# Performance work log

Hardware: AMD Instinct MI355X
Metric: run time of the kernel (lower is better)

The kernel has to match this reference:

```python
import jax, jax.numpy as jnp
import numpy as np

H, N, OUT = 1024, 64, 512  # channels, SSM state size, output feats


def posenc3d(f, h, w, channels):
    # standard positional_encodings.PositionalEncoding3D
    ch = int(np.ceil(channels / 6) * 2)  # per-axis channels (342 for 1024)
    inv_freq = jnp.asarray(1.0 / (10000.0 ** (np.arange(0, ch, 2, dtype=np.float32) / ch)))

    def emb(n):
        s = jnp.arange(n, dtype=jnp.float32)[:, None] * inv_freq[None, :]  # (n, ch/2)
        return jnp.stack([jnp.sin(s), jnp.cos(s)], axis=-1).reshape(n, -1)  # interleaved (n, ch)

    ex, ey, ez = emb(f), emb(h), emb(w)
    pe = jnp.zeros((f, h, w, ch * 3), dtype=jnp.float32)
    pe = pe.at[..., :ch].set(ex[:, None, None, :])
    pe = pe.at[..., ch:2 * ch].set(ey[None, :, None, :])
    pe = pe.at[..., 2 * ch:].set(ez[None, None, :, :])
    return pe[..., :channels]  # truncate 3*342=1026 -> 1024


def s4_kernel(log_dt, A_re, A_im, C_re, C_im, L):
    # S4D ZOH kernel: K[h,l] = 2*Re( sum_n C'[h,n] * exp(dt_h*A[h,n]*l) )
    dt = jnp.exp(log_dt)                      # (H,)
    A = A_re + 1j * A_im                      # (H,N)
    C = C_re + 1j * C_im                      # (H,N)
    dtA = dt[:, None] * A                     # (H,N)
    Ct = C * (jnp.exp(dtA) - 1.0) / A         # discretized C' (H,N)
    l = jnp.arange(L, dtype=jnp.float32)

    def body(acc, xs):  # scan over state dim to avoid (H,N,L) materialization
        ct, da = xs  # (H,), (H,)
        return acc + ct[:, None] * jnp.exp(da[:, None] * l), None

    acc0 = jnp.zeros((log_dt.shape[0], L), dtype=jnp.complex64)
    K, _ = jax.lax.scan(body, acc0, (Ct.T, dtA.T))
    return 2.0 * K.real  # (H, L)


def reference(x, log_dt, A_re, A_im, C_re, C_im, D, W_out, b_out):
    bs, ch, f, h, w = x.shape
    L = f * h * w
    u = jnp.transpose(x, (0, 2, 3, 4, 1))                 # bs f h w ch
    u = u + posenc3d(f, h, w, ch)[None]
    u = u.reshape(bs, L, ch)
    v = jnp.transpose(u, (0, 2, 1))                       # (bs, ch, L)
    K = s4_kernel(log_dt, A_re, A_im, C_re, C_im, L)      # (ch, L)
    # causal FFT convolution (pad to 2L)
    Uf = jnp.fft.rfft(v, 2 * L)
    Kf = jnp.fft.rfft(K, 2 * L)
    y = jnp.fft.irfft(Uf * Kf[None], 2 * L)[..., :L]
    y = y + D[None, :, None] * v                          # skip connection
    y = jax.nn.gelu(jnp.transpose(y, (0, 2, 1)))          # (bs, L, ch)
    out = y @ W_out + b_out                               # (bs, L, OUT)
    return jnp.transpose(out, (0, 2, 1)).reshape(bs, W_out.shape[1], f, h, w)


def setup_inputs() -> dict:
    key = jax.random.key(0)
    ks = jax.random.split(key, 6)
    bs, f, h, w = 2, 16, 16, 16
    x = jax.random.normal(ks[0], (bs, H, f, h, w), dtype=jnp.float32)
    # S4D-Lin init
    log_dt = jax.random.uniform(ks[1], (H,), dtype=jnp.float32) * (np.log(0.1) - np.log(0.001)) + np.log(0.001)
    A_re = -0.5 * jnp.ones((H, N), dtype=jnp.float32)
    A_im = jnp.broadcast_to(np.pi * jnp.arange(N, dtype=jnp.float32)[None, :], (H, N)).copy()
    C_re = jax.random.normal(ks[2], (H, N), dtype=jnp.float32) * (0.5 ** 0.5)
    C_im = jax.random.normal(ks[3], (H, N), dtype=jnp.float32) * (0.5 ** 0.5)
    D = jax.random.normal(ks[4], (H,), dtype=jnp.float32)
    W_out = jax.random.normal(ks[5], (H, OUT), dtype=jnp.float32) / np.float32(np.sqrt(H))
    b_out = jnp.zeros((OUT,), dtype=jnp.float32)
    return {"x": x, "log_dt": log_dt, "A_re": A_re, "A_im": A_im, "C_re": C_re,
            "C_im": C_im, "D": D, "W_out": W_out, "b_out": b_out}
```

## Files before the change

kernel.cpp:

```cpp
#include <hip/hip_runtime.h>
#include <cstdint>
#include <cstddef>

#define H_CH 1024
#define OUTF 512
#define LSEQ 4096

typedef __bf16 bf16x8 __attribute__((ext_vector_type(8)));
typedef float floatx4 __attribute__((ext_vector_type(4)));

__device__ __forceinline__ unsigned short f2bf(float f) {
    __bf16 b = (__bf16)f;
    return __builtin_bit_cast(unsigned short, b);
}
__device__ __forceinline__ unsigned int pack2(float a, float b) {
    return (unsigned int)f2bf(a) | ((unsigned int)f2bf(b) << 16);
}
__device__ __forceinline__ float bf2f(unsigned short u) {
    unsigned int x = ((unsigned int)u) << 16;
    return __builtin_bit_cast(float, x);
}
struct c32 { float x, y; };
__device__ __forceinline__ c32 cmul(c32 a, c32 b) {
    return { fmaf(a.x, b.x, -a.y * b.y), fmaf(a.x, b.y, a.y * b.x) };
}
__device__ __forceinline__ c32 cpow16(c32 a, int w) {
    c32 p = {1.f, 0.f};
    if (w) {
        c32 a2 = cmul(a, a), a4 = cmul(a2, a2), a8 = cmul(a4, a4), a16 = cmul(a8, a8);
        p = a16;
        for (int k = 1; k < w; ++k) p = cmul(p, a16);
    }
    return p;
}
__device__ __forceinline__ float gelu_fast(float y) {
    float u = y + 0.044715f * y * y * y;
    float e = __expf(-1.5957691216057308f * u);
    return y * __builtin_amdgcn_rcpf(1.f + e);
}

__global__ __launch_bounds__(256) void coef_kernel(
    const float* __restrict__ log_dt, const float* __restrict__ A_re,
    const float* __restrict__ A_im, const float* __restrict__ C_re,
    const float* __restrict__ C_im, float* __restrict__ coef)
{
    const int i = blockIdx.x * 256 + threadIdx.x;
    const int c = i >> 6;
    double are = A_re[i], aim = A_im[i], cre = C_re[i], cim = C_im[i];
    double dt  = exp((double)log_dt[c]);
    double dar = dt * are, dai = dt * aim;
    double er = exp(dar), cd = cos(dai), sd = sin(dai);
    double lre = er * cd, limm = er * sd;
    double ei = exp(-dar);
    double eQ = exp(64.0 * dar), cQ = cos(64.0 * dai), sQ = sin(64.0 * dai);
    double nre = lre - 1.0, nim = limm;
    double d2  = are * are + aim * aim;
    double qre = (nre * are + nim * aim) / d2;
    double qim = (nim * are - nre * aim) / d2;
    double ctre = cre * qre - cim * qim, ctim = cre * qim + cim * qre;
    float4 w0 = make_float4((float)lre, (float)limm, (float)(ei * cd), (float)(-ei * sd));
    float4 w1 = make_float4((float)(eQ * cQ), (float)(eQ * sQ),
                            (float)(2.0 * ctre), (float)(-2.0 * ctim));
    *(float4*)&coef[(size_t)i * 8]     = w0;
    *(float4*)&coef[(size_t)i * 8 + 4] = w1;
}

__global__ __launch_bounds__(256) void s4_fused_kernel(
    const float* __restrict__ x, const float* __restrict__ coef,
    const float* __restrict__ Dp, unsigned short* __restrict__ g)
{
    __shared__ __align__(16) unsigned short Vs[64 * 72];
    __shared__ __align__(16) unsigned short Ps[65 * 136];
    __shared__ __align__(16) unsigned char  RY[128 * 72 * 2];
    __shared__ __align__(16) unsigned short Ss[64 * 136];
    __shared__ __align__(16) unsigned short Ts[64 * 72];
    __shared__ float2 Es[4][64];
    __shared__ float  pe16[16];
    unsigned short* Fs   = (unsigned short*)RY;
    unsigned short* Rs   = (unsigned short*)RY;
    unsigned int*   ybuf = (unsigned int*)RY;

    const int c = blockIdx.x;
    const int t = threadIdx.x, lane = t & 63, w = t >> 6, n = lane;
    const int lm = lane & 15, lq = lane >> 4;

    const int axis = (c >= 684) ? 2 : ((c >= 342) ? 1 : 0);
    const int j = c - 342 * axis;
    const int is_cos = j & 1;
    if (t < 16) {
        const float freq = (float)exp(-log(10000.0) * (double)(2 * (j >> 1)) / 342.0);
        float a = (float)t * freq;
        pe16[t] = is_cos ? cosf(a) : sinf(a);
    }
    const float* cf = coef + ((size_t)c * 64 + n) * 8;
    c32 lam = {cf[0], cf[1]}, inv = {cf[2], cf[3]}, lamQ = {cf[4], cf[5]};
    const float c2r = cf[6], c2mi = cf[7];
    const float Dc = Dp[c];
    __syncthreads();

    auto deltascan = [&](int bb) {
        const float* xp = x + ((size_t)bb * H_CH + c) * (size_t)LSEQ;
        #pragma unroll
        for (int r = 0; r < 2; ++r) {
            const int i = r * 256 + t, l0 = i * 8;
            float4 f0 = *(const float4*)(xp + l0);
            float4 f1 = *(const float4*)(xp + l0 + 4);
            float e[8] = {f0.x, f0.y, f0.z, f0.w, f1.x, f1.y, f1.z, f1.w};
            unsigned int o[4];
            #pragma unroll
            for (int k = 0; k < 4; ++k) {
                const int la = l0 + 2 * k, lb = la + 1;
                const int pa = axis == 0 ? (la >> 8) : axis == 1 ? ((la >> 4) & 15) : (la & 15);
                const int pb = axis == 0 ? (lb >> 8) : axis == 1 ? ((lb >> 4) & 15) : (lb & 15);
                o[k] = pack2(e[2 * k] + pe16[pa], e[2 * k + 1] + pe16[pb]);
            }
            *(uint4*)&Vs[(i >> 3) * 72 + (i & 7) * 8] = make_uint4(o[0], o[1], o[2], o[3]);
        }
        {
            c32 l2 = cmul(lam, lam), l4 = cmul(l2, l2), l8 = cmul(l4, l4);
            c32 l16 = cmul(l8, l8), l32 = cmul(l16, l16);
            c32 z = cmul(cmul(cmul(cmul(cmul(l32, l16), l8), l4), l2), lam);
            z = cmul(z, cpow16(inv, w));
            #pragma unroll
            for (int s = 0; s < 16; ++s) {
                const int u = 16 * w + s;
                Fs[(2 * n) * 72 + u]     = f2bf(z.x);
                Fs[(2 * n + 1) * 72 + u] = f2bf(z.y);
                z = cmul(z, inv);
            }
        }
        __syncthreads();
        {
            floatx4 acc[2][4];
            #pragma unroll
            for (int a = 0; a < 2; ++a)
                #pragma unroll
                for (int b = 0; b < 4; ++b) acc[a][b] = (floatx4){0.f, 0.f, 0.f, 0.f};
            #pragma unroll
            for (int kt = 0; kt < 2; ++kt) {
                bf16x8 a0 = *(const bf16x8*)&Fs[(32 * w + lm) * 72 + kt * 32 + lq * 8];
                bf16x8 a1 = *(const bf16x8*)&Fs[(32 * w + 16 + lm) * 72 + kt * 32 + lq * 8];
                #pragma unroll
                for (int nt = 0; nt < 4; ++nt) {
                    bf16x8 b = *(const bf16x8*)&Vs[(nt * 16 + lm) * 72 + kt * 32 + lq * 8];
                    acc[0][nt] = __builtin_amdgcn_mfma_f32_16x16x32_bf16(a0, b, acc[0][nt], 0, 0, 0);
                    acc[1][nt] = __builtin_amdgcn_mfma_f32_16x16x32_bf16(a1, b, acc[1][nt], 0, 0, 0);
                }
            }
            #pragma unroll
            for (int sm = 0; sm < 2; ++sm)
                #pragma unroll
                for (int nt = 0; nt < 4; ++nt) {
                    const int row = 32 * w + sm * 16 + lq * 4, col = nt * 16 + lm;
                    *(uint2*)&Ss[col * 136 + row] =
                        make_uint2(pack2(acc[sm][nt][0], acc[sm][nt][1]),
                                   pack2(acc[sm][nt][2], acc[sm][nt][3]));
                }
        }
        __syncthreads();
        {
            float sr = 0.f, si = 0.f;
            #pragma unroll
            for (int jc = 0; jc < 16; ++jc) {
                unsigned int d = *(unsigned int*)&Ss[(16 * w + jc) * 136 + 2 * n];
                float dr = bf2f((unsigned short)(d & 0xffff));
                float di = bf2f((unsigned short)(d >> 16));
                float nr = fmaf(lamQ.x, sr, fmaf(-lamQ.y, si, dr));
                float ni = fmaf(lamQ.x, si, fmaf(lamQ.y, sr, di));
                sr = nr; si = ni;
            }
            Es[w][n] = make_float2(sr, si);
        }
        __syncthreads();
        {
            c32 Q2 = cmul(lamQ, lamQ), Q4 = cmul(Q2, Q2), Q8 = cmul(Q4, Q4);
            c32 Q16 = cmul(Q8, Q8);
            float cr = 0.f, ci = 0.f;
            for (int w2 = 0; w2 < w; ++w2) {
                float2 e = Es[w2][n];
                float nr = fmaf(Q16.x, cr, fmaf(-Q16.y, ci, e.x));
                float ni = fmaf(Q16.x, ci, fmaf(Q16.y, cr, e.y));
                cr = nr; ci = ni;
            }
            float sr = cr, si = ci;
            #pragma unroll
            for (int jc = 0; jc < 16; ++jc) {
                unsigned int* p = (unsigned int*)&Ss[(16 * w + jc) * 136 + 2 * n];
                unsigned int d = *p;
                *p = pack2(sr, si);
                float dr = bf2f((unsigned short)(d & 0xffff));
                float di = bf2f((unsigned short)(d >> 16));
                float nr = fmaf(lamQ.x, sr, fmaf(-lamQ.y, si, dr));
                float ni = fmaf(lamQ.x, si, fmaf(lamQ.y, sr, di));
                sr = nr; si = ni;
            }
        }
        __syncthreads();
    };

    auto gemm2_epi = [&](int bb) {
        floatx4 a2[4];
        #pragma unroll
        for (int nt = 0; nt < 4; ++nt) a2[nt] = (floatx4){0.f, 0.f, 0.f, 0.f};
        #pragma unroll
        for (int kt = 0; kt < 2; ++kt) {
            bf16x8 a = *(const bf16x8*)&Ts[(16 * w + lm) * 72 + kt * 32 + lq * 8];
            #pragma unroll
            for (int nt = 0; nt < 4; ++nt) {
                bf16x8 b = *(const bf16x8*)&Vs[(nt * 16 + lm) * 72 + kt * 32 + lq * 8];
                a2[nt] = __builtin_amdgcn_mfma_f32_16x16x32_bf16(a, b, a2[nt], 0, 0, 0);
            }
        }
        #pragma unroll
        for (int kt = 0; kt < 4; ++kt) {
            bf16x8 a = *(const bf16x8*)&Ps[(16 * w + lm + 1) * 136 + kt * 32 + lq * 8];
            #pragma unroll
            for (int nt = 0; nt < 4; ++nt) {
                bf16x8 b = *(const bf16x8*)&Ss[(nt * 16 + lm) * 136 + kt * 32 + lq * 8];
                a2[nt] = __builtin_amdgcn_mfma_f32_16x16x32_bf16(a, b, a2[nt], 0, 0, 0);
            }
        }
        __syncthreads();
        #pragma unroll
        for (int nt = 0; nt < 4; ++nt) {
            const int chunk = nt * 16 + lm;
            float gg[4];
            #pragma unroll
            for (int r = 0; r < 4; ++r) {
                const int tt = 16 * w + lq * 4 + r;
                const float vv = bf2f(Vs[chunk * 72 + tt]);
                gg[r] = gelu_fast(fmaf(Dc, vv, a2[nt][r]));
            }
            const int p0 = 8 * w + 2 * lq;
            ybuf[chunk * 34 + p0]     = pack2(gg[0], gg[1]);
            ybuf[chunk * 34 + p0 + 1] = pack2(gg[2], gg[3]);
        }
        __syncthreads();
        unsigned int* gp = (unsigned int*)(g + ((size_t)bb * H_CH + c) * (size_t)LSEQ);
        #pragma unroll
        for (int q = 0; q < 8; ++q) {
            const int idx = q * 256 + t;
            gp[idx] = ybuf[(idx >> 5) * 34 + (idx & 31)];
        }
        __syncthreads();
    };

    deltascan(0);

    {
        c32 z = cmul((c32){c2r, -c2mi}, cpow16(lam, w));
        const int steps = (w == 3) ? 17 : 16;
        for (int s = 0; s < steps; ++s) {
            const int tt = 16 * w + s;
            *(unsigned int*)&Ps[tt * 136 + 2 * n] = pack2(z.x, -z.y);
            z = cmul(z, lam);
        }
    }
    {
        c32 z = cpow16(inv, w);
        #pragma unroll
        for (int s = 0; s < 16; ++s) {
            const int u = 16 * w + s;
            *(unsigned int*)&Rs[u * 136 + 2 * n] = pack2(z.x, z.y);
            z = cmul(z, inv);
        }
    }
    __syncthreads();
    {
        floatx4 a1[4];
        #pragma unroll
        for (int nt = 0; nt < 4; ++nt) a1[nt] = (floatx4){0.f, 0.f, 0.f, 0.f};
        #pragma unroll
        for (int kt = 0; kt < 4; ++kt) {
            bf16x8 a = *(const bf16x8*)&Ps[(16 * w + lm) * 136 + kt * 32 + lq * 8];
            #pragma unroll
            for (int nt = 0; nt < 4; ++nt) {
                bf16x8 b = *(const bf16x8*)&Rs[(nt * 16 + lm) * 136 + kt * 32 + lq * 8];
                a1[nt] = __builtin_amdgcn_mfma_f32_16x16x32_bf16(a, b, a1[nt], 0, 0, 0);
            }
        }
        #pragma unroll
        for (int nt = 0; nt < 4; ++nt)
            #pragma unroll
            for (int r = 0; r < 4; ++r) {
                const int row = 16 * w + lq * 4 + r, col = nt * 16 + lm;
                Ts[row * 72 + col] = f2bf(row >= col ? a1[nt][r] : 0.f);
            }
    }
    __syncthreads();

    gemm2_epi(0);
    deltascan(1);
    gemm2_epi(1);
}

__global__ __launch_bounds__(256) void transpose_g_kernel(
    const unsigned short* __restrict__ g_bcl, unsigned short* __restrict__ gT)
{
    __shared__ unsigned int tileU[64 * 33];
    const int t = threadIdx.x, ty = t >> 5, tx = t & 31;
    const int l0 = blockIdx.x * 64, c0 = blockIdx.y * 64, b = blockIdx.z;
    #pragma unroll
    for (int r = 0; r < 8; ++r) {
        const int ci = r * 8 + ty;
        tileU[ci * 33 + tx] =
            *(const unsigned int*)&g_bcl[((size_t)b * H_CH + c0 + ci) * LSEQ + l0 + tx * 2];
    }
    __syncthreads();
    #pragma unroll
    for (int r = 0; r < 8; ++r) {
        const int li = r * 8 + ty;
        unsigned int ua = tileU[(2 * tx) * 33 + (li >> 1)];
        unsigned int ub = tileU[(2 * tx + 1) * 33 + (li >> 1)];
        unsigned int s0 = (li & 1) ? (ua >> 16) : (ua & 0xffffu);
        unsigned int s1 = (li & 1) ? (ub >> 16) : (ub & 0xffffu);
        *(unsigned int*)&gT[((size_t)b * LSEQ + l0 + li) * H_CH + c0 + 2 * tx] =
            s0 | (s1 << 16);
    }
}

__global__ __launch_bounds__(256) void transpose_w_kernel(
    const float* __restrict__ W, unsigned short* __restrict__ Wt)
{
    __shared__ float tileF[64 * 65];
    const int t = threadIdx.x;
    const int o0 = blockIdx.x * 64, k0 = blockIdx.y * 64;
    {
        const int ty = t >> 6, tx = t & 63;
        #pragma unroll
        for (int r = 0; r < 16; ++r) {
            const int ki = r * 4 + ty;
            tileF[ki * 65 + tx] = W[(size_t)(k0 + ki) * OUTF + o0 + tx];
        }
    }
    __syncthreads();
    {
        const int ty = t >> 5, tx = t & 31;
        #pragma unroll
        for (int r = 0; r < 8; ++r) {
            const int oi = r * 8 + ty;
            unsigned int u0 = f2bf(tileF[(2 * tx) * 65 + oi]);
            unsigned int u1 = f2bf(tileF[(2 * tx + 1) * 65 + oi]);
            *(unsigned int*)&Wt[(size_t)(o0 + oi) * H_CH + k0 + 2 * tx] = u0 | (u1 << 16);
        }
    }
}

__global__ __launch_bounds__(256) void gemm_kernel(
    const unsigned short* __restrict__ gT, const unsigned short* __restrict__ Wt,
    const float* __restrict__ b_out, float* __restrict__ out)
{
    __shared__ unsigned short As[128 * 40];
    __shared__ unsigned short Bs[128 * 40];
    const int t = threadIdx.x, lane = t & 63, wid = t >> 6;
    const int wo = wid & 1, wl = wid >> 1;
    const int lm = lane & 15, lq = lane >> 4;
    const int l0 = blockIdx.x * 128, o0 = blockIdx.y * 128, bb = blockIdx.z;
    const unsigned short* gB = gT + (size_t)bb * LSEQ * H_CH;

    floatx4 acc[4][4];
    #pragma unroll
    for (int i = 0; i < 4; ++i)
        #pragma unroll
        for (int jj = 0; jj < 4; ++jj) acc[i][jj] = (floatx4){0.f, 0.f, 0.f, 0.f};

    for (int kt = 0; kt < 32; ++kt) {
        const int k0 = kt * 32;
        __syncthreads();
        #pragma unroll
        for (int half = 0; half < 2; ++half) {
            const int chunk = t + half * 256;
            const int row = chunk >> 2, q = chunk & 3;
            *(uint4*)&As[row * 40 + q * 8] =
                *(const uint4*)(Wt + (size_t)(o0 + row) * H_CH + k0 + q * 8);
            *(uint4*)&Bs[row * 40 + q * 8] =
                *(const uint4*)(gB + (size_t)(l0 + row) * H_CH + k0 + q * 8);
        }
        __syncthreads();

        bf16x8 af[4], bfr[4];
        #pragma unroll
        for (int sm = 0; sm < 4; ++sm)
            af[sm] = *(const bf16x8*)&As[(wo * 64 + sm * 16 + lm) * 40 + lq * 8];
        #pragma unroll
        for (int sn = 0; sn < 4; ++sn)
            bfr[sn] = *(const bf16x8*)&Bs[(wl * 64 + sn * 16 + lm) * 40 + lq * 8];
        #pragma unroll
        for (int sm = 0; sm < 4; ++sm)
            #pragma unroll
            for (int sn = 0; sn < 4; ++sn)
                acc[sm][sn] = __builtin_amdgcn_mfma_f32_16x16x32_bf16(
                    af[sm], bfr[sn], acc[sm][sn], 0, 0, 0);
    }

    #pragma unroll
    for (int sm = 0; sm < 4; ++sm)
        #pragma unroll
        for (int sn = 0; sn < 4; ++sn)
            #pragma unroll
            for (int r = 0; r < 4; ++r) {
                const int o = o0 + wo * 64 + sm * 16 + lq * 4 + r;
                const int l = l0 + wl * 64 + sn * 16 + lm;
                out[((size_t)bb * OUTF + o) * LSEQ + l] = acc[sm][sn][r] + b_out[o];
            }
}

extern "C" void kernel_launch(void* const* d_in, const int* in_sizes, int n_in,
                              void* d_out, int out_size, void* d_ws, size_t ws_size,
                              hipStream_t stream) {
    const float* x      = (const float*)d_in[0];
    const float* log_dt = (const float*)d_in[1];
    const float* A_re   = (const float*)d_in[2];
    const float* A_im   = (const float*)d_in[3];
    const float* C_re   = (const float*)d_in[4];
    const float* C_im   = (const float*)d_in[5];
    const float* Dp     = (const float*)d_in[6];
    const float* W_out  = (const float*)d_in[7];
    const float* b_out  = (const float*)d_in[8];
    float* out = (float*)d_out;

    char* ws = (char*)d_ws;
    unsigned short* g    = (unsigned short*)ws;
    unsigned short* gT   = (unsigned short*)(ws + (size_t)16 * 1024 * 1024);
    unsigned short* Wt   = (unsigned short*)(ws + (size_t)32 * 1024 * 1024);
    float*          coef = (float*)(ws + (size_t)33 * 1024 * 1024);

    coef_kernel<<<256, 256, 0, stream>>>(log_dt, A_re, A_im, C_re, C_im, coef);
    s4_fused_kernel<<<1024, 256, 0, stream>>>(x, coef, Dp, g);
    transpose_g_kernel<<<dim3(64, 16, 2), 256, 0, stream>>>(g, gT);
    transpose_w_kernel<<<dim3(8, 16), 256, 0, stream>>>(W_out, Wt);
    gemm_kernel<<<dim3(32, 4, 2), 256, 0, stream>>>(gT, Wt, b_out, out);
}
```

Measured before the change: 147.7 us.

## Write g in GEMM-tiled layout and drop the separate transpose kernel

```diff
diff --git a/kernel.cpp b/kernel.cpp
--- a/kernel.cpp
+++ b/kernel.cpp
@@ -67,7 +67,7 @@
 
 __global__ __launch_bounds__(256) void s4_fused_kernel(
     const float* __restrict__ x, const float* __restrict__ coef,
-    const float* __restrict__ Dp, unsigned short* __restrict__ g)
+    const float* __restrict__ Dp, unsigned short* __restrict__ gprime)
 {
     __shared__ __align__(16) unsigned short Vs[64 * 72];
     __shared__ __align__(16) unsigned short Ps[65 * 136];
@@ -236,11 +236,13 @@
             ybuf[chunk * 34 + p0 + 1] = pack2(gg[2], gg[3]);
         }
         __syncthreads();
-        unsigned int* gp = (unsigned int*)(g + ((size_t)bb * H_CH + c) * (size_t)LSEQ);
+        unsigned int* gp = (unsigned int*)gprime
+                         + (size_t)bb * 32 * 1024 * 64 + (size_t)c * 64;
         #pragma unroll
         for (int q = 0; q < 8; ++q) {
             const int idx = q * 256 + t;
-            gp[idx] = ybuf[(idx >> 5) * 34 + (idx & 31)];
+            const int lt = idx >> 6, w32 = idx & 63;
+            gp[(size_t)lt * (1024 * 64) + w32] = ybuf[(idx >> 5) * 34 + (idx & 31)];
         }
         __syncthreads();
     };
@@ -294,31 +296,6 @@
     gemm2_epi(1);
 }
 
-__global__ __launch_bounds__(256) void transpose_g_kernel(
-    const unsigned short* __restrict__ g_bcl, unsigned short* __restrict__ gT)
-{
-    __shared__ unsigned int tileU[64 * 33];
-    const int t = threadIdx.x, ty = t >> 5, tx = t & 31;
-    const int l0 = blockIdx.x * 64, c0 = blockIdx.y * 64, b = blockIdx.z;
-    #pragma unroll
-    for (int r = 0; r < 8; ++r) {
-        const int ci = r * 8 + ty;
-        tileU[ci * 33 + tx] =
-            *(const unsigned int*)&g_bcl[((size_t)b * H_CH + c0 + ci) * LSEQ + l0 + tx * 2];
-    }
-    __syncthreads();
-    #pragma unroll
-    for (int r = 0; r < 8; ++r) {
-        const int li = r * 8 + ty;
-        unsigned int ua = tileU[(2 * tx) * 33 + (li >> 1)];
-        unsigned int ub = tileU[(2 * tx + 1) * 33 + (li >> 1)];
-        unsigned int s0 = (li & 1) ? (ua >> 16) : (ua & 0xffffu);
-        unsigned int s1 = (li & 1) ? (ub >> 16) : (ub & 0xffffu);
-        *(unsigned int*)&gT[((size_t)b * LSEQ + l0 + li) * H_CH + c0 + 2 * tx] =
-            s0 | (s1 << 16);
-    }
-}
-
 __global__ __launch_bounds__(256) void transpose_w_kernel(
     const float* __restrict__ W, unsigned short* __restrict__ Wt)
 {
@@ -347,48 +324,71 @@
 }
 
 __global__ __launch_bounds__(256) void gemm_kernel(
-    const unsigned short* __restrict__ gT, const unsigned short* __restrict__ Wt,
+    const unsigned short* __restrict__ gp, const unsigned short* __restrict__ Wt,
     const float* __restrict__ b_out, float* __restrict__ out)
 {
-    __shared__ unsigned short As[128 * 40];
+    __shared__ unsigned short As[64 * 40];
     __shared__ unsigned short Bs[128 * 40];
-    const int t = threadIdx.x, lane = t & 63, wid = t >> 6;
-    const int wo = wid & 1, wl = wid >> 1;
+    const int t = threadIdx.x, lane = t & 63, w = t >> 6;
     const int lm = lane & 15, lq = lane >> 4;
-    const int l0 = blockIdx.x * 128, o0 = blockIdx.y * 128, bb = blockIdx.z;
-    const unsigned short* gB = gT + (size_t)bb * LSEQ * H_CH;
-
-    floatx4 acc[4][4];
+    const int bx = blockIdx.x;
+    const int o0 = blockIdx.y * 64;
+    const int bb = blockIdx.z;
+    const int l0 = bx * 128;
+    const unsigned short* bsrc = gp + (size_t)(bb * 32 + bx) * (1024 * 128);
+
+    const int arow = t >> 2, aq = t & 3;
+    const int bp = t & 15, bgq = t >> 4;
+
+    uint4 areg, breg0, breg1;
+    {
+        areg  = *(const uint4*)(Wt + (size_t)(o0 + arow) * H_CH + aq * 8);
+        const unsigned short* b0 = bsrc + (size_t)(2 * bp) * 128 + bgq * 8;
+        breg0 = *(const uint4*)(b0);
+        breg1 = *(const uint4*)(b0 + 128);
+    }
+
+    floatx4 acc[4][2];
     #pragma unroll
     for (int i = 0; i < 4; ++i)
         #pragma unroll
-        for (int jj = 0; jj < 4; ++jj) acc[i][jj] = (floatx4){0.f, 0.f, 0.f, 0.f};
+        for (int jj = 0; jj < 2; ++jj) acc[i][jj] = (floatx4){0.f, 0.f, 0.f, 0.f};
 
     for (int kt = 0; kt < 32; ++kt) {
-        const int k0 = kt * 32;
-        __syncthreads();
-        #pragma unroll
-        for (int half = 0; half < 2; ++half) {
-            const int chunk = t + half * 256;
-            const int row = chunk >> 2, q = chunk & 3;
-            *(uint4*)&As[row * 40 + q * 8] =
-                *(const uint4*)(Wt + (size_t)(o0 + row) * H_CH + k0 + q * 8);
-            *(uint4*)&Bs[row * 40 + q * 8] =
-                *(const uint4*)(gB + (size_t)(l0 + row) * H_CH + k0 + q * 8);
-        }
-        __syncthreads();
-
-        bf16x8 af[4], bfr[4];
+        if (kt) __syncthreads();
+        *(uint4*)&As[arow * 40 + aq * 8] = areg;
+        {
+            unsigned int* bu = (unsigned int*)Bs;
+            const unsigned int* a = (const unsigned int*)&breg0;
+            const unsigned int* b = (const unsigned int*)&breg1;
+            #pragma unroll
+            for (int i = 0; i < 4; ++i) {
+                unsigned int lo = (a[i] & 0xffffu) | (b[i] << 16);
+                unsigned int hi = (a[i] >> 16) | (b[i] & 0xffff0000u);
+                bu[(bgq * 8 + 2 * i) * 20 + bp]     = lo;
+                bu[(bgq * 8 + 2 * i + 1) * 20 + bp] = hi;
+            }
+        }
+        __syncthreads();
+        if (kt < 31) {
+            const int k0 = (kt + 1) * 32;
+            areg  = *(const uint4*)(Wt + (size_t)(o0 + arow) * H_CH + k0 + aq * 8);
+            const unsigned short* b0 = bsrc + (size_t)(k0 + 2 * bp) * 128 + bgq * 8;
+            breg0 = *(const uint4*)(b0);
+            breg1 = *(const uint4*)(b0 + 128);
+        }
+
+        bf16x8 af[4], bfr[2];
         #pragma unroll
         for (int sm = 0; sm < 4; ++sm)
-            af[sm] = *(const bf16x8*)&As[(wo * 64 + sm * 16 + lm) * 40 + lq * 8];
-        #pragma unroll
-        for (int sn = 0; sn < 4; ++sn)
-            bfr[sn] = *(const bf16x8*)&Bs[(wl * 64 + sn * 16 + lm) * 40 + lq * 8];
+            af[sm] = *(const bf16x8*)&As[(sm * 16 + lm) * 40 + lq * 8];
+        #pragma unroll
+        for (int sn = 0; sn < 2; ++sn)
+            bfr[sn] = *(const bf16x8*)&Bs[(w * 32 + sn * 16 + lm) * 40 + lq * 8];
         #pragma unroll
         for (int sm = 0; sm < 4; ++sm)
             #pragma unroll
-            for (int sn = 0; sn < 4; ++sn)
+            for (int sn = 0; sn < 2; ++sn)
                 acc[sm][sn] = __builtin_amdgcn_mfma_f32_16x16x32_bf16(
                     af[sm], bfr[sn], acc[sm][sn], 0, 0, 0);
     }
@@ -396,11 +396,11 @@
     #pragma unroll
     for (int sm = 0; sm < 4; ++sm)
         #pragma unroll
-        for (int sn = 0; sn < 4; ++sn)
+        for (int sn = 0; sn < 2; ++sn)
             #pragma unroll
             for (int r = 0; r < 4; ++r) {
-                const int o = o0 + wo * 64 + sm * 16 + lq * 4 + r;
-                const int l = l0 + wl * 64 + sn * 16 + lm;
+                const int o = o0 + sm * 16 + lq * 4 + r;
+                const int l = l0 + w * 32 + sn * 16 + lm;
                 out[((size_t)bb * OUTF + o) * LSEQ + l] = acc[sm][sn][r] + b_out[o];
             }
 }
@@ -420,14 +420,12 @@
     float* out = (float*)d_out;
 
     char* ws = (char*)d_ws;
-    unsigned short* g    = (unsigned short*)ws;
-    unsigned short* gT   = (unsigned short*)(ws + (size_t)16 * 1024 * 1024);
-    unsigned short* Wt   = (unsigned short*)(ws + (size_t)32 * 1024 * 1024);
-    float*          coef = (float*)(ws + (size_t)33 * 1024 * 1024);
+    unsigned short* gprime = (unsigned short*)ws;
+    unsigned short* Wt     = (unsigned short*)(ws + (size_t)17 * 1024 * 1024);
+    float*          coef   = (float*)(ws + (size_t)19 * 1024 * 1024);
 
     coef_kernel<<<256, 256, 0, stream>>>(log_dt, A_re, A_im, C_re, C_im, coef);
-    s4_fused_kernel<<<1024, 256, 0, stream>>>(x, coef, Dp, g);
-    transpose_g_kernel<<<dim3(64, 16, 2), 256, 0, stream>>>(g, gT);
+    s4_fused_kernel<<<1024, 256, 0, stream>>>(x, coef, Dp, gprime);
     transpose_w_kernel<<<dim3(8, 16), 256, 0, stream>>>(W_out, Wt);
-    gemm_kernel<<<dim3(32, 4, 2), 256, 0, stream>>>(gT, Wt, b_out, out);
-}
+    gemm_kernel<<<dim3(32, 8, 2), 256, 0, stream>>>(gprime, Wt, b_out, out);
+}
```

Result: no change. 146.4 us (-0.9%).
